# Kernel optimization log

Measured on AMD Instinct MI355X. Metric: run time of the kernel, lower is better.

The kernel has to match this reference:

```python
import jax, jax.numpy as jnp
import numpy as np

L = 12; NH = 12; DH = 64; H = 768; FF = 3072; S = 1024; B = 4; V = 50265; WIN = 256  # one-sided window (attention_window=512)

def _ln(x, g, b, eps=1e-5):
    m = jnp.mean(x, axis=-1, keepdims=True)
    v = jnp.mean((x - m) ** 2, axis=-1, keepdims=True)
    return (x - m) * jax.lax.rsqrt(v + eps) * g + b

def _local_attn(q, k, v, mask, w):
    # q,k,v: [B,NH,S,DH]; mask: [B,S] ints (1=attend, 0=pad).
    # Sliding-window attention computed in query blocks of size w over key spans of 3w
    # (no global tokens: forward never passes a global_attention_mask).
    b, nh, s, dh = q.shape
    c = w; nb = s // c; span = 3 * c
    qb = q.reshape(b, nh, nb, c, dh)
    kp = jnp.pad(k, ((0, 0), (0, 0), (w, w), (0, 0)))
    vp = jnp.pad(v, ((0, 0), (0, 0), (w, w), (0, 0)))
    idx = jnp.arange(nb)[:, None] * c + jnp.arange(span)[None, :]  # [nb, span]
    kb = kp[:, :, idx]  # [B,NH,nb,span,DH]
    vb = vp[:, :, idx]
    scores = jnp.einsum('bhncd,bhnkd->bhnck', qb, kb) / np.float32(np.sqrt(dh))
    qi = jnp.arange(c)[:, None]; kj = jnp.arange(span)[None, :]
    band = (kj - qi >= 0) & (kj - qi <= 2 * w)  # |k_abs - q_abs| <= w
    mp = jnp.pad(mask, ((0, 0), (w, w)))  # zero pad also masks out-of-range keys
    mb = mp[:, idx] > 0  # [B, nb, span]
    ok = band[None, None, None, :, :] & mb[:, None, :, None, :]
    scores = jnp.where(ok, scores, jnp.float32(-1e9))
    probs = jax.nn.softmax(scores, axis=-1)
    out = jnp.einsum('bhnck,bhnkd->bhncd', probs, vb)
    return out.reshape(b, nh, s, dh)

def _forward(WE, PE, Eg, Eb, Wq, bq, Wk, bk, Wv, bv, Wo, bo, g1, beta1, W1, b1, W2, b2, g2, beta2, aw, Wc, bc, input_ids, attention_mask):
    b, s = input_ids.shape
    h = WE[input_ids] + PE[jnp.arange(s)]
    h = _ln(h, Eg, Eb)
    for l in range(L):
        q = (h @ Wq[l] + bq[l]).reshape(b, s, NH, DH).transpose(0, 2, 1, 3)
        k = (h @ Wk[l] + bk[l]).reshape(b, s, NH, DH).transpose(0, 2, 1, 3)
        v = (h @ Wv[l] + bv[l]).reshape(b, s, NH, DH).transpose(0, 2, 1, 3)
        a = _local_attn(q, k, v, attention_mask, WIN)
        a = a.transpose(0, 2, 1, 3).reshape(b, s, H) @ Wo[l] + bo[l]
        h = _ln(h + a, g1[l], beta1[l])
        f = jax.nn.gelu(h @ W1[l] + b1[l], approximate=False) @ W2[l] + b2[l]
        h = _ln(h + f, g2[l], beta2[l])
    # attention-pooling head: softmax over seq of h @ aw, weighted sum, linear classifier
    sc = h @ aw  # [B,S]
    probs = jax.nn.softmax(sc, axis=1)
    pooled = jnp.sum(h * probs[..., None], axis=1)  # [B,H]
    return pooled @ Wc + bc  # [B,1] (dropout is identity in eval)

def setup_inputs():
    key = jax.random.key(0)
    ks = jax.random.split(key, 16)
    n = lambda k, shape: 0.02 * jax.random.normal(k, shape, dtype=jnp.float32)
    return {
        'WE': n(ks[0], (V, H)), 'PE': n(ks[1], (S, H)),
        'Eg': jnp.ones((H,), jnp.float32), 'Eb': jnp.zeros((H,), jnp.float32),
        'Wq': n(ks[2], (L, H, H)), 'bq': jnp.zeros((L, H), jnp.float32),
        'Wk': n(ks[3], (L, H, H)), 'bk': jnp.zeros((L, H), jnp.float32),
        'Wv': n(ks[4], (L, H, H)), 'bv': jnp.zeros((L, H), jnp.float32),
        'Wo': n(ks[5], (L, H, H)), 'bo': jnp.zeros((L, H), jnp.float32),
        'g1': jnp.ones((L, H), jnp.float32), 'beta1': jnp.zeros((L, H), jnp.float32),
        'W1': n(ks[6], (L, H, FF)), 'b1': jnp.zeros((L, FF), jnp.float32),
        'W2': n(ks[7], (L, FF, H)), 'b2': jnp.zeros((L, H), jnp.float32),
        'g2': jnp.ones((L, H), jnp.float32), 'beta2': jnp.zeros((L, H), jnp.float32),
        'aw': jax.random.normal(ks[8], (H,), dtype=jnp.float32),
        'Wc': n(ks[9], (H, 1)), 'bc': jnp.zeros((1,), jnp.float32),
        'input_ids': jax.random.randint(ks[10], (B, S), 0, V, dtype=jnp.int32),
        'attention_mask': jnp.ones((B, S), jnp.int32),
    }

def reference(WE, PE, Eg, Eb, Wq, bq, Wk, bk, Wv, bv, Wo, bo, g1, beta1, W1, b1, W2, b2, g2, beta2, aw, Wc, bc, input_ids, attention_mask):
    return _forward(WE, PE, Eg, Eb, Wq, bq, Wk, bk, Wv, bv, Wo, bo, g1, beta1, W1, b1, W2, b2, g2, beta2, aw, Wc, bc, input_ids, attention_mask)
```

## Files before the change

kernel.cpp:

```cpp
#include <hip/hip_runtime.h>
#include <hip/hip_bf16.h>

#define LAYERS 12
#define NHEAD  12
#define DHEAD  64
#define HDIM   768
#define FFDIM  3072
#define SEQ    1024
#define BATCH  4
#define WINSZ  256
#define MTOK   (BATCH*SEQ)
#define PLANE  ((size_t)MTOK*HDIM)

typedef unsigned short u16;
typedef unsigned int   u32;

using f32x4  = __attribute__((ext_vector_type(4))) float;
using bf16x8 = __attribute__((ext_vector_type(8))) short;

__device__ __forceinline__ float bflo(u32 u){ union{u32 i;float f;}x; x.i = u << 16; return x.f; }
__device__ __forceinline__ float bfhi(u32 u){ union{u32 i;float f;}x; x.i = u & 0xffff0000u; return x.f; }
__device__ __forceinline__ u16 f2bf(float f){
    union{float f;u32 u;}x; x.f = f;
    u32 r = x.u + 0x7fffu + ((x.u >> 16) & 1u);
    return (u16)(r >> 16);
}
__device__ __forceinline__ void gload16(const u16* g, u16* l) {
    __builtin_amdgcn_global_load_lds(
        (const __attribute__((address_space(1))) u32*)g,
        (__attribute__((address_space(3))) u32*)l, 16, 0, 0);
}

__device__ __forceinline__ float wave_sum(float v) {
#pragma unroll
    for (int o = 32; o > 0; o >>= 1) v += __shfl_down(v, o, 64);
    return v;
}
__device__ __forceinline__ float wave_max(float v) {
#pragma unroll
    for (int o = 32; o > 0; o >>= 1) v = fmaxf(v, __shfl_down(v, o, 64));
    return v;
}
__device__ __forceinline__ float blk_sum256(float v, float* sm) {
    v = wave_sum(v);
    int lane = threadIdx.x & 63, w = threadIdx.x >> 6;
    __syncthreads();
    if (lane == 0) sm[w] = v;
    __syncthreads();
    return sm[0] + sm[1] + sm[2] + sm[3];
}
__device__ __forceinline__ float blk_sum1024(float v, float* sm) {
    v = wave_sum(v);
    int lane = threadIdx.x & 63, w = threadIdx.x >> 6;
    __syncthreads();
    if (lane == 0) sm[w] = v;
    __syncthreads();
    float r = 0.f;
#pragma unroll
    for (int i = 0; i < 16; i++) r += sm[i];
    return r;
}
__device__ __forceinline__ float blk_max1024(float v, float* sm) {
    v = wave_max(v);
    int lane = threadIdx.x & 63, w = threadIdx.x >> 6;
    __syncthreads();
    if (lane == 0) sm[w] = v;
    __syncthreads();
    float r = -1e30f;
#pragma unroll
    for (int i = 0; i < 16; i++) r = fmaxf(r, sm[i]);
    return r;
}

__global__ __launch_bounds__(256) void k_embed_ln(
    const float* __restrict__ WE, const float* __restrict__ PE,
    const float* __restrict__ g, const float* __restrict__ bta,
    const int* __restrict__ ids, float* __restrict__ h, u16* __restrict__ hb)
{
    __shared__ float sm[4];
    int tok = blockIdx.x;
    int s = tok & (SEQ - 1);
    int id = ids[tok];
    int tt = threadIdx.x;
    float4 x = make_float4(0.f, 0.f, 0.f, 0.f);
    if (tt < HDIM / 4) {
        float4 a = ((const float4*)(WE + (size_t)id * HDIM))[tt];
        float4 b = ((const float4*)(PE + (size_t)s * HDIM))[tt];
        x = make_float4(a.x + b.x, a.y + b.y, a.z + b.z, a.w + b.w);
    }
    float s1 = blk_sum256(x.x + x.y + x.z + x.w, sm);
    float s2 = blk_sum256(x.x*x.x + x.y*x.y + x.z*x.z + x.w*x.w, sm);
    float mean = s1 * (1.f / HDIM);
    float var  = s2 * (1.f / HDIM) - mean * mean;
    float inv  = rsqrtf(var + 1e-5f);
    if (tt < HDIM / 4) {
        float4 gg = ((const float4*)g)[tt];
        float4 bb = ((const float4*)bta)[tt];
        float4 o;
        o.x = (x.x - mean) * inv * gg.x + bb.x;
        o.y = (x.y - mean) * inv * gg.y + bb.y;
        o.z = (x.z - mean) * inv * gg.z + bb.z;
        o.w = (x.w - mean) * inv * gg.w + bb.w;
        ((float4*)(h + (size_t)tok * HDIM))[tt] = o;
        uint2 pk;
        pk.x = (u32)f2bf(o.x) | ((u32)f2bf(o.y) << 16);
        pk.y = (u32)f2bf(o.z) | ((u32)f2bf(o.w) << 16);
        ((uint2*)(hb + (size_t)tok * HDIM))[tt] = pk;
    }
}

__global__ __launch_bounds__(256) void k_addln(
    float* __restrict__ h, const float* __restrict__ t,
    const float* __restrict__ g, const float* __restrict__ bta, u16* __restrict__ hb)
{
    __shared__ float sm[4];
    int tok = blockIdx.x;
    int tt = threadIdx.x;
    float4 x = make_float4(0.f, 0.f, 0.f, 0.f);
    if (tt < HDIM / 4) {
        float4 a = ((const float4*)(h + (size_t)tok * HDIM))[tt];
        float4 b = ((const float4*)(t + (size_t)tok * HDIM))[tt];
        x = make_float4(a.x + b.x, a.y + b.y, a.z + b.z, a.w + b.w);
    }
    float s1 = blk_sum256(x.x + x.y + x.z + x.w, sm);
    float s2 = blk_sum256(x.x*x.x + x.y*x.y + x.z*x.z + x.w*x.w, sm);
    float mean = s1 * (1.f / HDIM);
    float var  = s2 * (1.f / HDIM) - mean * mean;
    float inv  = rsqrtf(var + 1e-5f);
    if (tt < HDIM / 4) {
        float4 gg = ((const float4*)g)[tt];
        float4 bb = ((const float4*)bta)[tt];
        float4 o;
        o.x = (x.x - mean) * inv * gg.x + bb.x;
        o.y = (x.y - mean) * inv * gg.y + bb.y;
        o.z = (x.z - mean) * inv * gg.z + bb.z;
        o.w = (x.w - mean) * inv * gg.w + bb.w;
        ((float4*)(h + (size_t)tok * HDIM))[tt] = o;
        uint2 pk;
        pk.x = (u32)f2bf(o.x) | ((u32)f2bf(o.y) << 16);
        pk.y = (u32)f2bf(o.z) | ((u32)f2bf(o.w) << 16);
        ((uint2*)(hb + (size_t)tok * HDIM))[tt] = pk;
    }
}

__global__ __launch_bounds__(256) void k_cvtT(
    const float* __restrict__ W, u16* __restrict__ dst, int K, int N,
    size_t ss, size_t ds)
{
    __shared__ float t[32][33];
    W   += (size_t)blockIdx.z * ss;
    dst += (size_t)blockIdx.z * ds;
    int n0 = blockIdx.x * 32, k0 = blockIdx.y * 32;
    int c = threadIdx.x & 31, r8 = threadIdx.x >> 5;
#pragma unroll
    for (int p = 0; p < 4; p++) {
        int k = r8 + p * 8;
        t[k][c] = W[(size_t)(k0 + k) * N + n0 + c];
    }
    __syncthreads();
#pragma unroll
    for (int p = 0; p < 2; p++) {
        int idx = threadIdx.x + p * 256;
        int n = idx >> 4, kp = idx & 15;
        float a = t[kp*2][n], b = t[kp*2+1][n];
        u32 pk = (u32)f2bf(a) | ((u32)f2bf(b) << 16);
        u32* d = (u32*)(dst + (size_t)(n0 + n) * K + k0);
        d[kp] = pk;
    }
}

template<int BM, int BN, int MODE>
__global__ __launch_bounds__(256) void k_gemm_mfma(
    const u16* __restrict__ A, const u16* __restrict__ BT,
    const float* __restrict__ b0, const float* __restrict__ b1, const float* __restrict__ b2,
    void* __restrict__ C, int K, int N)
{
    __shared__ u16 As[BM * 32];
    __shared__ u16 Bs[BN * 32];
    const int tid = threadIdx.x, lane = tid & 63, w = tid >> 6;
    const int bm = blockIdx.y * BM, bn = blockIdx.x * BN;
    constexpr int MT = BM / 32, NT = BN / 32;
    constexpr int AR = BM / 4, BR = BN / 4;
    constexpr int AI = AR / 16, BI = BR / 16;
    const int wm = (w & 1) * (BM / 2), wn = (w >> 1) * (BN / 2);

    f32x4 acc[MT][NT];
#pragma unroll
    for (int mi = 0; mi < MT; mi++)
#pragma unroll
        for (int ni = 0; ni < NT; ni++) acc[mi][ni] = (f32x4){0.f, 0.f, 0.f, 0.f};

    const u16* ag = A  + (size_t)(bm + w * AR + (lane >> 2)) * K + (lane & 3) * 8;
    const u16* bg = BT + (size_t)(bn + w * BR + (lane >> 2)) * K + (lane & 3) * 8;
    u16* al = As + w * AR * 32;
    u16* bl = Bs + w * BR * 32;
    const int fr = lane & 15, fq = (lane >> 4) * 8;

    for (int k0 = 0; k0 < K; k0 += 32) {
#pragma unroll
        for (int i = 0; i < AI; i++) gload16(ag + (size_t)i * 16 * K + k0, al + i * 512);
#pragma unroll
        for (int i = 0; i < BI; i++) gload16(bg + (size_t)i * 16 * K + k0, bl + i * 512);
        __syncthreads();
        bf16x8 af[MT], bf[NT];
#pragma unroll
        for (int mi = 0; mi < MT; mi++)
            af[mi] = *(const bf16x8*)(As + (wm + mi * 16 + fr) * 32 + fq);
#pragma unroll
        for (int ni = 0; ni < NT; ni++)
            bf[ni] = *(const bf16x8*)(Bs + (wn + ni * 16 + fr) * 32 + fq);
#pragma unroll
        for (int mi = 0; mi < MT; mi++)
#pragma unroll
            for (int ni = 0; ni < NT; ni++)
                acc[mi][ni] = __builtin_amdgcn_mfma_f32_16x16x32_bf16(af[mi], bf[ni], acc[mi][ni], 0, 0, 0);
        __syncthreads();
    }

#pragma unroll
    for (int mi = 0; mi < MT; mi++) {
        int m_base = bm + wm + mi * 16 + (lane >> 4) * 4;
#pragma unroll
        for (int ni = 0; ni < NT; ni++) {
            int n_g = bn + wn + ni * 16 + (lane & 15);
            const float* bp = b0; int nn = n_g; int which = 0;
            if (MODE == 1) {
                if (n_g >= 1536)      { bp = b2; nn = n_g - 1536; which = 2; }
                else if (n_g >= 768)  { bp = b1; nn = n_g - 768;  which = 1; }
            }
            float bias = bp[nn];
#pragma unroll
            for (int r = 0; r < 4; r++) {
                int m_g = m_base + r;
                float val = acc[mi][ni][r] + bias;
                if (MODE == 0) {
                    ((float*)C)[(size_t)m_g * N + n_g] = val;
                } else if (MODE == 1) {
                    int bb = m_g >> 10, ss = m_g & 1023;
                    int hh = nn >> 6, dd = nn & 63;
                    ((u16*)C)[(size_t)which * PLANE + (((size_t)bb * NHEAD + hh) * SEQ + ss) * DHEAD + dd] = f2bf(val);
                } else {
                    val = 0.5f * val * (1.f + erff(val * 0.70710678118f));
                    ((u16*)C)[(size_t)m_g * N + n_g] = f2bf(val);
                }
            }
        }
    }
}

#define PADW 72
__global__ __launch_bounds__(256) void k_attn_mfma(
    const u16* __restrict__ qkv, const int* __restrict__ mask, u16* __restrict__ abuf)
{
    __shared__ u16 Qs[64 * PADW];
    __shared__ u16 Ks[64 * PADW];
    __shared__ u16 Vt[64 * PADW];
    __shared__ u16 Ps[64 * PADW];
    __shared__ int ms[64];
    const int tid = threadIdx.x, lane = tid & 63, w = tid >> 6;
    int blk = blockIdx.x;
    int qt = blk & 15;
    int hh = (blk >> 4) % NHEAD;
    int b  = blk / (16 * NHEAD);
    int q0 = qt * 64;

    const u16* qp = qkv + ((size_t)b * NHEAD + hh) * SEQ * DHEAD;
    const u16* kp = qp + PLANE;
    const u16* vp = qp + 2 * PLANE;

#pragma unroll
    for (int it = 0; it < 2; it++) {
        int idx = tid + it * 256;
        int r = idx >> 3, c8 = (idx & 7) * 8;
        uint4 u = *(const uint4*)(qp + (size_t)(q0 + r) * DHEAD + c8);
        *(uint4*)(Qs + r * PADW + c8) = u;
    }

    const int fr = lane & 15, g4 = (lane >> 4) * 4, fq = (lane >> 4) * 8;
    const int wq = w * 16;
    const int qpos = q0 + wq + g4;

    f32x4 o[4];
#pragma unroll
    for (int d = 0; d < 4; d++) o[d] = (f32x4){0.f, 0.f, 0.f, 0.f};
    float mr[4], ll[4];
#pragma unroll
    for (int r = 0; r < 4; r++) { mr[r] = -1e9f; ll[r] = 0.f; }

    __syncthreads();
    bf16x8 aq[2];
#pragma unroll
    for (int ks = 0; ks < 2; ks++)
        aq[ks] = *(const bf16x8*)(Qs + (wq + fr) * PADW + ks * 32 + fq);

    for (int ch = 0; ch < 9; ch++) {
        int kbase = q0 - 256 + ch * 64;
        __syncthreads();
#pragma unroll
        for (int it = 0; it < 2; it++) {
            int idx = tid + it * 256;
            int r = idx >> 3, c8 = (idx & 7) * 8;
            int kq = kbase + r;
            uint4 u = (kq >= 0 && kq < SEQ)
                ? *(const uint4*)(kp + (size_t)kq * DHEAD + c8)
                : make_uint4(0u, 0u, 0u, 0u);
            *(uint4*)(Ks + r * PADW + c8) = u;
        }
        {
            int r = tid >> 2, sg = (tid & 3) * 16;
            int kq = kbase + r;
            uint4 u0 = make_uint4(0u,0u,0u,0u), u1 = u0;
            if (kq >= 0 && kq < SEQ) {
                const uint4* vr = (const uint4*)(vp + (size_t)kq * DHEAD + sg);
                u0 = vr[0]; u1 = vr[1];
            }
            u32 ww[8] = {u0.x, u0.y, u0.z, u0.w, u1.x, u1.y, u1.z, u1.w};
#pragma unroll
            for (int j = 0; j < 8; j++) {
                Vt[(sg + 2*j    ) * PADW + r] = (u16)(ww[j] & 0xffffu);
                Vt[(sg + 2*j + 1) * PADW + r] = (u16)(ww[j] >> 16);
            }
        }
        if (tid < 64) {
            int kq = kbase + tid;
            ms[tid] = (kq >= 0 && kq < SEQ) ? mask[b * SEQ + kq] : 0;
        }
        __syncthreads();

        f32x4 s[4];
#pragma unroll
        for (int nt = 0; nt < 4; nt++) s[nt] = (f32x4){0.f, 0.f, 0.f, 0.f};
#pragma unroll
        for (int nt = 0; nt < 4; nt++)
#pragma unroll
            for (int ks = 0; ks < 2; ks++) {
                bf16x8 bk = *(const bf16x8*)(Ks + (nt*16 + fr) * PADW + ks*32 + fq);
                s[nt] = __builtin_amdgcn_mfma_f32_16x16x32_bf16(aq[ks], bk, s[nt], 0, 0, 0);
            }

        float mloc[4];
#pragma unroll
        for (int r = 0; r < 4; r++) mloc[r] = -1e9f;
#pragma unroll
        for (int nt = 0; nt < 4; nt++) {
            int kpos = kbase + nt*16 + fr;
            int msv = ms[nt*16 + fr];
#pragma unroll
            for (int r = 0; r < 4; r++) {
                int dq = kpos - (qpos + r);
                bool ok = (dq >= -WINSZ) && (dq <= WINSZ) && (msv != 0);
                float sv = ok ? s[nt][r] * 0.125f : -1e9f;
                s[nt][r] = sv;
                mloc[r] = fmaxf(mloc[r], sv);
            }
        }
#pragma unroll
        for (int mk = 1; mk < 16; mk <<= 1)
#pragma unroll
            for (int r = 0; r < 4; r++)
                mloc[r] = fmaxf(mloc[r], __shfl_xor(mloc[r], mk, 64));

        float sc4[4], psum[4];
#pragma unroll
        for (int r = 0; r < 4; r++) {
            float mn = fmaxf(mr[r], mloc[r]);
            sc4[r] = __expf(mr[r] - mn);
            mr[r] = mn;
            psum[r] = 0.f;
        }
#pragma unroll
        for (int nt = 0; nt < 4; nt++)
#pragma unroll
            for (int r = 0; r < 4; r++) {
                float p = (s[nt][r] > -1e8f) ? __expf(s[nt][r] - mr[r]) : 0.f;
                psum[r] += p;
                Ps[(wq + g4 + r) * PADW + nt*16 + fr] = f2bf(p);
            }
#pragma unroll
        for (int mk = 1; mk < 16; mk <<= 1)
#pragma unroll
            for (int r = 0; r < 4; r++)
                psum[r] += __shfl_xor(psum[r], mk, 64);

        f32x4 scv = (f32x4){sc4[0], sc4[1], sc4[2], sc4[3]};
#pragma unroll
        for (int r = 0; r < 4; r++) ll[r] = ll[r] * sc4[r] + psum[r];
#pragma unroll
        for (int d = 0; d < 4; d++) o[d] *= scv;

#pragma unroll
        for (int ks = 0; ks < 2; ks++) {
            bf16x8 ap = *(const bf16x8*)(Ps + (wq + fr) * PADW + ks*32 + fq);
#pragma unroll
            for (int d = 0; d < 4; d++) {
                bf16x8 bv8 = *(const bf16x8*)(Vt + (d*16 + fr) * PADW + ks*32 + fq);
                o[d] = __builtin_amdgcn_mfma_f32_16x16x32_bf16(ap, bv8, o[d], 0, 0, 0);
            }
        }
    }

#pragma unroll
    for (int r = 0; r < 4; r++) {
        float inv = 1.f / ll[r];
        u16* orow = abuf + ((size_t)(b * SEQ + q0 + wq + g4 + r)) * HDIM + hh * DHEAD;
#pragma unroll
        for (int d = 0; d < 4; d++)
            orow[d*16 + fr] = f2bf(o[d][r] * inv);
    }
}

__global__ __launch_bounds__(1024) void k_pool(
    const float* __restrict__ h, const float* __restrict__ aw,
    const float* __restrict__ Wc, const float* __restrict__ bc,
    float* __restrict__ out)
{
    __shared__ float aws[HDIM];
    __shared__ float ps[SEQ];
    __shared__ float red[16];
    int b = blockIdx.x;
    for (int d = threadIdx.x; d < HDIM; d += 1024) aws[d] = aw[d];
    __syncthreads();
    const float* hb = h + (size_t)b * SEQ * HDIM;
    int s = threadIdx.x;
    float sc = 0.f;
    const float4* hr = (const float4*)(hb + (size_t)s * HDIM);
#pragma unroll 4
    for (int c = 0; c < HDIM / 4; c++) {
        float4 x = hr[c];
        sc += x.x * aws[4*c] + x.y * aws[4*c+1] + x.z * aws[4*c+2] + x.w * aws[4*c+3];
    }
    float mx = blk_max1024(sc, red);
    float e = __expf(sc - mx);
    float tot = blk_sum1024(e, red);
    ps[s] = e / tot;
    __syncthreads();
    float outv = 0.f;
    if (threadIdx.x < HDIM) {
        int d = threadIdx.x;
        float pd = 0.f;
        for (int ss = 0; ss < SEQ; ss++) pd += hb[(size_t)ss * HDIM + d] * ps[ss];
        outv = pd * Wc[d];
    }
    float total = blk_sum1024(outv, red);
    if (threadIdx.x == 0) out[b] = total + bc[0];
}

extern "C" void kernel_launch(void* const* d_in, const int* in_sizes, int n_in,
                              void* d_out, int out_size, void* d_ws, size_t ws_size,
                              hipStream_t stream)
{
    const float* WE    = (const float*)d_in[0];
    const float* PE    = (const float*)d_in[1];
    const float* Eg    = (const float*)d_in[2];
    const float* Eb    = (const float*)d_in[3];
    const float* Wq    = (const float*)d_in[4];
    const float* bq    = (const float*)d_in[5];
    const float* Wk    = (const float*)d_in[6];
    const float* bk    = (const float*)d_in[7];
    const float* Wv    = (const float*)d_in[8];
    const float* bv    = (const float*)d_in[9];
    const float* Wo    = (const float*)d_in[10];
    const float* bo    = (const float*)d_in[11];
    const float* g1    = (const float*)d_in[12];
    const float* beta1 = (const float*)d_in[13];
    const float* W1    = (const float*)d_in[14];
    const float* b1    = (const float*)d_in[15];
    const float* W2    = (const float*)d_in[16];
    const float* b2    = (const float*)d_in[17];
    const float* g2    = (const float*)d_in[18];
    const float* beta2 = (const float*)d_in[19];
    const float* aw    = (const float*)d_in[20];
    const float* Wc    = (const float*)d_in[21];
    const float* bc    = (const float*)d_in[22];
    const int* ids     = (const int*)d_in[23];
    const int* msk     = (const int*)d_in[24];

    char* base = (char*)d_ws;
    float* h    = (float*)base;                               base += (size_t)MTOK * HDIM * 4;
    float* tbuf = (float*)base;                               base += (size_t)MTOK * HDIM * 4;
    u16*   hb   = (u16*)base;                                 base += (size_t)MTOK * HDIM * 2;
    u16*   X    = (u16*)base;                                 base += (size_t)MTOK * FFDIM * 2;
    u16*   qkv  = X;
    u16*   abuf = X + 3 * PLANE;
    u16*   mid  = X;

    const size_t sQKV = (size_t)2304 * HDIM;
    const size_t sWO  = (size_t)HDIM * HDIM;
    const size_t sW1  = (size_t)FFDIM * HDIM;
    const size_t sW2  = (size_t)HDIM * FFDIM;
    size_t fixed = (size_t)(base - (char*)d_ws);
    size_t all_bytes = fixed + (size_t)LAYERS * (sQKV + sWO + sW1 + sW2) * 2;
    bool wsall = ws_size >= all_bytes;
    int NL = wsall ? LAYERS : 1;
    u16* wqkvT = (u16*)base;
    u16* woT   = wqkvT + sQKV * NL;
    u16* w1T   = woT   + sWO  * NL;
    u16* w2T   = w1T   + sW1  * NL;

    k_embed_ln<<<MTOK, 256, 0, stream>>>(WE, PE, Eg, Eb, ids, h, hb);

    if (wsall) {
        k_cvtT<<<dim3(24, 24, LAYERS), 256, 0, stream>>>(Wq, wqkvT,                     HDIM, HDIM, (size_t)HDIM*HDIM, sQKV);
        k_cvtT<<<dim3(24, 24, LAYERS), 256, 0, stream>>>(Wk, wqkvT + (size_t)HDIM*HDIM, HDIM, HDIM, (size_t)HDIM*HDIM, sQKV);
        k_cvtT<<<dim3(24, 24, LAYERS), 256, 0, stream>>>(Wv, wqkvT + (size_t)2*HDIM*HDIM, HDIM, HDIM, (size_t)HDIM*HDIM, sQKV);
        k_cvtT<<<dim3(24, 24, LAYERS), 256, 0, stream>>>(Wo, woT, HDIM, HDIM, (size_t)HDIM*HDIM, sWO);
        k_cvtT<<<dim3(96, 24, LAYERS), 256, 0, stream>>>(W1, w1T, HDIM, FFDIM, (size_t)HDIM*FFDIM, sW1);
        k_cvtT<<<dim3(24, 96, LAYERS), 256, 0, stream>>>(W2, w2T, FFDIM, HDIM, (size_t)FFDIM*HDIM, sW2);
    }

    for (int l = 0; l < LAYERS; l++) {
        u16* wqkvT_l = wqkvT + (wsall ? (size_t)l * sQKV : 0);
        u16* woT_l   = woT   + (wsall ? (size_t)l * sWO  : 0);
        u16* w1T_l   = w1T   + (wsall ? (size_t)l * sW1  : 0);
        u16* w2T_l   = w2T   + (wsall ? (size_t)l * sW2  : 0);

        if (!wsall) {
            const float* Wql = Wq + (size_t)l * HDIM * HDIM;
            const float* Wkl = Wk + (size_t)l * HDIM * HDIM;
            const float* Wvl = Wv + (size_t)l * HDIM * HDIM;
            const float* Wol = Wo + (size_t)l * HDIM * HDIM;
            const float* W1l = W1 + (size_t)l * HDIM * FFDIM;
            const float* W2l = W2 + (size_t)l * FFDIM * HDIM;
            k_cvtT<<<dim3(24, 24), 256, 0, stream>>>(Wql, wqkvT_l,                      HDIM, HDIM, 0, 0);
            k_cvtT<<<dim3(24, 24), 256, 0, stream>>>(Wkl, wqkvT_l + (size_t)HDIM*HDIM,  HDIM, HDIM, 0, 0);
            k_cvtT<<<dim3(24, 24), 256, 0, stream>>>(Wvl, wqkvT_l + (size_t)2*HDIM*HDIM,HDIM, HDIM, 0, 0);
            k_cvtT<<<dim3(24, 24), 256, 0, stream>>>(Wol, woT_l, HDIM, HDIM, 0, 0);
            k_cvtT<<<dim3(96, 24), 256, 0, stream>>>(W1l, w1T_l, HDIM, FFDIM, 0, 0);
            k_cvtT<<<dim3(24, 96), 256, 0, stream>>>(W2l, w2T_l, FFDIM, HDIM, 0, 0);
        }

        k_gemm_mfma<128, 128, 1><<<dim3(2304/128, MTOK/128), 256, 0, stream>>>(
            hb, wqkvT_l, bq + l*HDIM, bk + l*HDIM, bv + l*HDIM, qkv, HDIM, 2304);
        k_attn_mfma<<<BATCH * NHEAD * (SEQ/64), 256, 0, stream>>>(qkv, msk, abuf);
        k_gemm_mfma<128, 64, 0><<<dim3(HDIM/64, MTOK/128), 256, 0, stream>>>(
            abuf, woT_l, bo + l*HDIM, nullptr, nullptr, tbuf, HDIM, HDIM);
        k_addln<<<MTOK, 256, 0, stream>>>(h, tbuf, g1 + l*HDIM, beta1 + l*HDIM, hb);
        k_gemm_mfma<128, 128, 2><<<dim3(FFDIM/128, MTOK/128), 256, 0, stream>>>(
            hb, w1T_l, b1 + l*FFDIM, nullptr, nullptr, mid, HDIM, FFDIM);
        k_gemm_mfma<128, 64, 0><<<dim3(HDIM/64, MTOK/128), 256, 0, stream>>>(
            mid, w2T_l, b2 + l*HDIM, nullptr, nullptr, tbuf, FFDIM, HDIM);
        k_addln<<<MTOK, 256, 0, stream>>>(h, tbuf, g2 + l*HDIM, beta2 + l*HDIM, hb);
    }

    k_pool<<<BATCH, 1024, 0, stream>>>(h, aw, Wc, bc, (float*)d_out);
}
```

Measured before the change: 3.037 ms.

## Split attention pooling into parallel score, softmax, reduce and final kernels

Replaces the single four-block pooling kernel with four kernels. One wave per token computes the scores, each batch gets its own softmax block, the weighted sum over tokens is split into 16 chunks per batch, and a final kernel combines the chunks with the classifier weights. The goal is to spread the large read of the hidden states across many blocks instead of four. In exchange it adds three kernel launches and a partial-sum buffer stored in the reused tbuf scratch.

New measurement: 2.939 ms. 3.2% less time.

```diff
diff --git a/kernel.cpp b/kernel.cpp
--- a/kernel.cpp
+++ b/kernel.cpp
@@ -409,40 +409,72 @@
     }
 }
 
-__global__ __launch_bounds__(1024) void k_pool(
-    const float* __restrict__ h, const float* __restrict__ aw,
-    const float* __restrict__ Wc, const float* __restrict__ bc,
-    float* __restrict__ out)
-{
-    __shared__ float aws[HDIM];
-    __shared__ float ps[SEQ];
+__global__ __launch_bounds__(256) void k_pool_score(
+    const float* __restrict__ h, const float* __restrict__ aw, float* __restrict__ sc)
+{
+    int tok = blockIdx.x * 4 + (threadIdx.x >> 6);
+    int lane = threadIdx.x & 63;
+    const float4* hr = (const float4*)(h + (size_t)tok * HDIM);
+    const float4* ar = (const float4*)aw;
+    float acc = 0.f;
+#pragma unroll
+    for (int i = 0; i < 3; i++) {
+        int c = lane + i * 64;
+        float4 x = hr[c], a = ar[c];
+        acc += x.x*a.x + x.y*a.y + x.z*a.z + x.w*a.w;
+    }
+    acc = wave_sum(acc);
+    if (lane == 0) sc[tok] = acc;
+}
+
+__global__ __launch_bounds__(1024) void k_pool_softmax(float* __restrict__ sc)
+{
     __shared__ float red[16];
     int b = blockIdx.x;
-    for (int d = threadIdx.x; d < HDIM; d += 1024) aws[d] = aw[d];
-    __syncthreads();
-    const float* hb = h + (size_t)b * SEQ * HDIM;
-    int s = threadIdx.x;
-    float sc = 0.f;
-    const float4* hr = (const float4*)(hb + (size_t)s * HDIM);
-#pragma unroll 4
-    for (int c = 0; c < HDIM / 4; c++) {
-        float4 x = hr[c];
-        sc += x.x * aws[4*c] + x.y * aws[4*c+1] + x.z * aws[4*c+2] + x.w * aws[4*c+3];
-    }
-    float mx = blk_max1024(sc, red);
-    float e = __expf(sc - mx);
+    float v = sc[b * SEQ + threadIdx.x];
+    float mx = blk_max1024(v, red);
+    float e = __expf(v - mx);
     float tot = blk_sum1024(e, red);
-    ps[s] = e / tot;
-    __syncthreads();
-    float outv = 0.f;
-    if (threadIdx.x < HDIM) {
-        int d = threadIdx.x;
+    sc[b * SEQ + threadIdx.x] = e / tot;
+}
+
+__global__ __launch_bounds__(256) void k_pool_reduce(
+    const float* __restrict__ h, const float* __restrict__ ps, float* __restrict__ partial)
+{
+    int b = blockIdx.x, j = blockIdx.y;
+    int tid = threadIdx.x;
+    const float* hb = h + ((size_t)b * SEQ + j * 64) * HDIM;
+    const float* pp = ps + b * SEQ + j * 64;
+    float a0 = 0.f, a1 = 0.f, a2 = 0.f;
+    for (int s = 0; s < 64; s++) {
+        float p = pp[s];
+        const float* row = hb + (size_t)s * HDIM;
+        a0 = fmaf(row[tid],       p, a0);
+        a1 = fmaf(row[tid + 256], p, a1);
+        a2 = fmaf(row[tid + 512], p, a2);
+    }
+    float* outp = partial + ((size_t)b * 16 + j) * HDIM;
+    outp[tid] = a0; outp[tid + 256] = a1; outp[tid + 512] = a2;
+}
+
+__global__ __launch_bounds__(256) void k_pool_final(
+    const float* __restrict__ partial, const float* __restrict__ Wc,
+    const float* __restrict__ bc, float* __restrict__ out)
+{
+    __shared__ float sm[4];
+    int b = blockIdx.x, tid = threadIdx.x;
+    float acc = 0.f;
+#pragma unroll
+    for (int dd = 0; dd < 3; dd++) {
+        int d = tid + dd * 256;
         float pd = 0.f;
-        for (int ss = 0; ss < SEQ; ss++) pd += hb[(size_t)ss * HDIM + d] * ps[ss];
-        outv = pd * Wc[d];
-    }
-    float total = blk_sum1024(outv, red);
-    if (threadIdx.x == 0) out[b] = total + bc[0];
+#pragma unroll
+        for (int j = 0; j < 16; j++)
+            pd += partial[((size_t)b * 16 + j) * HDIM + d];
+        acc = fmaf(pd, Wc[d], acc);
+    }
+    float total = blk_sum256(acc, sm);
+    if (tid == 0) out[b] = total + bc[0];
 }
 
 extern "C" void kernel_launch(void* const* d_in, const int* in_sizes, int n_in,
@@ -542,5 +574,10 @@
         k_addln<<<MTOK, 256, 0, stream>>>(h, tbuf, g2 + l*HDIM, beta2 + l*HDIM, hb);
     }
 
-    k_pool<<<BATCH, 1024, 0, stream>>>(h, aw, Wc, bc, (float*)d_out);
-}
+    float* ps      = tbuf;
+    float* partial = tbuf + BATCH * SEQ;
+    k_pool_score  <<<MTOK / 4, 256, 0, stream>>>(h, aw, ps);
+    k_pool_softmax<<<BATCH, 1024, 0, stream>>>(ps);
+    k_pool_reduce <<<dim3(BATCH, 16), 256, 0, stream>>>(h, ps, partial);
+    k_pool_final  <<<BATCH, 256, 0, stream>>>(partial, Wc, bc, (float*)d_out);
+}
```
